# Kernel tuning notes

Hardware: AMD Instinct MI355X
Metric: run time of the kernel (lower is better)

## Reference

```python
import jax, jax.numpy as jnp
import numpy as np

TOP_K = 2
EPS = 1e-10


def setup_inputs() -> dict:
    key = jax.random.key(0)
    k1, k2 = jax.random.split(key)
    B, S, D, E = 4, 4096, 4096, 64
    hidden_states = jax.random.normal(k1, (B, S, D), dtype=jnp.float32)
    # router weight, scaled like a standard linear init
    w_router = jax.random.normal(k2, (D, E), dtype=jnp.float32) / np.sqrt(D)
    return {"hidden_states": hidden_states, "w_router": w_router}


def reference(hidden_states, w_router):
    # router: [B,S,D] x [D,E] -> [B,S,E]
    router_logits = jnp.einsum("bsd,de->bse", hidden_states, w_router)
    # balanced_assignment: softmax, global load, penalty, adjusted top-k
    routing_probs = jax.nn.softmax(router_logits, axis=-1)
    current_load = routing_probs.sum(axis=(0, 1))            # [E]
    load_penalty = current_load / (current_load.mean() + EPS)  # [E]
    adjusted_logits = router_logits - jnp.log(load_penalty + EPS)
    _, expert_indices = jax.lax.top_k(adjusted_logits, TOP_K)  # [B,S,top_k]
    return adjusted_logits, expert_indices
```

## Files before the change

kernel.cpp:

```cpp
#include <hip/hip_runtime.h>
#include <math.h>

#define ROWS 16384
#define DD   4096
#define EE   64
#define EPSF 1e-10f

#define BM     128
#define KT     32
#define KSPLIT 4
#define KRANGE (DD / KSPLIT)
#define NKT    (KRANGE / KT)
#define HPAD   36

typedef __attribute__((ext_vector_type(8))) short short8;
typedef __attribute__((ext_vector_type(4))) float f32x4;

__device__ __forceinline__ short rne_bf16(float f) {
  unsigned u = __float_as_uint(f);
  return (short)((u + 0x7fffu + ((u >> 16) & 1u)) >> 16);
}
__device__ __forceinline__ float bf2f(short s) {
  return __uint_as_float(((unsigned)(unsigned short)s) << 16);
}
__device__ __forceinline__ void split3(float f, short& s0, short& s1,
                                       short& s2) {
  s0 = rne_bf16(f);
  float r1 = f - bf2f(s0);
  s1 = rne_bf16(r1);
  s2 = rne_bf16(r1 - bf2f(s1));
}

__global__ __launch_bounds__(256) void k_gemm(
    const float* __restrict__ h, const float* __restrict__ wr,
    float* __restrict__ logits) {
  __shared__ alignas(16) float hs[2][BM * HPAD];
  __shared__ alignas(16) short wsf[2][3][4][64][8];

  const int t = threadIdx.x;
  const int lane = t & 63;
  const int wv = t >> 6;
  const int row0 = (blockIdx.x >> 2) * BM;
  const int kb0 = (blockIdx.x & 3) * KRANGE;

  f32x4 acc[2][4] = {};

  const int hr = t >> 3;
  const int hk = (t & 7) * 4;
  const int we = lane;
  const int wq = wv;

  float4 hpf[4];
  float wpf[8];

  {
    const float* hp = h + (size_t)(row0 + hr) * DD + kb0 + hk;
#pragma unroll
    for (int i = 0; i < 4; ++i)
      hpf[i] = *(const float4*)(hp + (size_t)32 * i * DD);
    const float* wp = wr + (size_t)(kb0 + wq * 8) * EE + we;
#pragma unroll
    for (int j = 0; j < 8; ++j) wpf[j] = wp[(size_t)j * EE];
  }

  for (int kt = 0; kt < NKT; ++kt) {
    const int buf = kt & 1;
    __syncthreads();
#pragma unroll
    for (int i = 0; i < 4; ++i)
      *(float4*)&hs[buf][(hr + 32 * i) * HPAD + hk] = hpf[i];
    {
      short8 p0, p1, p2;
#pragma unroll
      for (int j = 0; j < 8; ++j) {
        short a, b, c;
        split3(wpf[j], a, b, c);
        p0[j] = a; p1[j] = b; p2[j] = c;
      }
      const int lp = wq * 16 + (we & 15);
      const int et = we >> 4;
      *(short8*)&wsf[buf][0][et][lp][0] = p0;
      *(short8*)&wsf[buf][1][et][lp][0] = p1;
      *(short8*)&wsf[buf][2][et][lp][0] = p2;
    }
    if (kt + 1 < NKT) {
      const int kb = kb0 + (kt + 1) * KT;
      const float* hp = h + (size_t)(row0 + hr) * DD + kb + hk;
#pragma unroll
      for (int i = 0; i < 4; ++i)
        hpf[i] = *(const float4*)(hp + (size_t)32 * i * DD);
      const float* wp = wr + (size_t)(kb + wq * 8) * EE + we;
#pragma unroll
      for (int j = 0; j < 8; ++j) wpf[j] = wp[(size_t)j * EE];
    }
    __syncthreads();

    short8 bf[3][4];
#pragma unroll
    for (int p = 0; p < 3; ++p)
#pragma unroll
      for (int et = 0; et < 4; ++et)
        bf[p][et] = *(const short8*)&wsf[buf][p][et][lane][0];

#pragma unroll
    for (int mt = 0; mt < 2; ++mt) {
      const int rl = wv * 32 + mt * 16 + (lane & 15);
      const float* ap = &hs[buf][rl * HPAD + (lane >> 4) * 8];
      float4 a0 = *(const float4*)ap;
      float4 a1 = *(const float4*)(ap + 4);
      float af[8] = {a0.x, a0.y, a0.z, a0.w, a1.x, a1.y, a1.z, a1.w};
      short8 ah0, ah1, ah2;
#pragma unroll
      for (int j = 0; j < 8; ++j) {
        short a, b, c;
        split3(af[j], a, b, c);
        ah0[j] = a; ah1[j] = b; ah2[j] = c;
      }
#pragma unroll
      for (int et = 0; et < 4; ++et) {
        f32x4 c = acc[mt][et];
        c = __builtin_amdgcn_mfma_f32_16x16x32_bf16(ah0, bf[0][et], c, 0, 0, 0);
        c = __builtin_amdgcn_mfma_f32_16x16x32_bf16(ah0, bf[1][et], c, 0, 0, 0);
        c = __builtin_amdgcn_mfma_f32_16x16x32_bf16(ah1, bf[0][et], c, 0, 0, 0);
        c = __builtin_amdgcn_mfma_f32_16x16x32_bf16(ah0, bf[2][et], c, 0, 0, 0);
        c = __builtin_amdgcn_mfma_f32_16x16x32_bf16(ah1, bf[1][et], c, 0, 0, 0);
        c = __builtin_amdgcn_mfma_f32_16x16x32_bf16(ah2, bf[0][et], c, 0, 0, 0);
        acc[mt][et] = c;
      }
    }
  }

#pragma unroll
  for (int mt = 0; mt < 2; ++mt) {
    const int rbase = row0 + wv * 32 + mt * 16 + (lane >> 4) * 4;
    const int col = lane & 15;
#pragma unroll
    for (int et = 0; et < 4; ++et) {
#pragma unroll
      for (int r = 0; r < 4; ++r)
        atomicAdd(&logits[(size_t)(rbase + r) * EE + et * 16 + col],
                  acc[mt][et][r]);
    }
  }
}

__global__ __launch_bounds__(256) void k_softload(
    const float* __restrict__ logits, float* __restrict__ g_load) {
  __shared__ float red[4][64];
  const int lane = threadIdx.x & 63;
  const int wv = threadIdx.x >> 6;
  float accp = 0.f;
#pragma unroll 4
  for (int i = 0; i < 32; ++i) {
    int row = blockIdx.x * 128 + wv * 32 + i;
    float x = logits[(size_t)row * EE + lane];
    float m = x;
#pragma unroll
    for (int off = 32; off > 0; off >>= 1) m = fmaxf(m, __shfl_xor(m, off, 64));
    float p = __expf(x - m);
    float s = p;
#pragma unroll
    for (int off = 32; off > 0; off >>= 1) s += __shfl_xor(s, off, 64);
    accp += p / s;
  }
  red[wv][lane] = accp;
  __syncthreads();
  if (wv == 0) {
    float s = red[0][lane] + red[1][lane] + red[2][lane] + red[3][lane];
    atomicAdd(&g_load[lane], s);
  }
}

__global__ void k_penalty(const float* __restrict__ g_load,
                          float* __restrict__ g_lp) {
  int t = threadIdx.x;
  float v = g_load[t];
  float s = v;
#pragma unroll
  for (int off = 32; off > 0; off >>= 1) s += __shfl_xor(s, off, 64);
  float mean = s * (1.f / 64.f);
  g_lp[t] = logf(v / (mean + EPSF) + EPSF);
}

__global__ __launch_bounds__(256) void k_top2(float* __restrict__ logits,
                                              const float* __restrict__ g_lp,
                                              float* __restrict__ idx_out) {
  int t = threadIdx.x;
  int lane = t & 63;
  int wv = t >> 6;
  int row = blockIdx.x * 4 + wv;
  size_t base = (size_t)row * EE;

  float a = logits[base + lane] - g_lp[lane];
  logits[base + lane] = a;

  float v = a;
  int idx = lane;
#pragma unroll
  for (int off = 32; off > 0; off >>= 1) {
    float ov = __shfl_xor(v, off, 64);
    int oi = __shfl_xor(idx, off, 64);
    if (ov > v || (ov == v && oi < idx)) { v = ov; idx = oi; }
  }
  int i1 = idx;

  float a2 = (lane == i1) ? -INFINITY : a;
  v = a2;
  idx = lane;
#pragma unroll
  for (int off = 32; off > 0; off >>= 1) {
    float ov = __shfl_xor(v, off, 64);
    int oi = __shfl_xor(idx, off, 64);
    if (ov > v || (ov == v && oi < idx)) { v = ov; idx = oi; }
  }
  int i2 = idx;

  if (lane == 0) {
    idx_out[(size_t)row * 2 + 0] = (float)i1;
    idx_out[(size_t)row * 2 + 1] = (float)i2;
  }
}

extern "C" void kernel_launch(void* const* d_in, const int* in_sizes, int n_in,
                              void* d_out, int out_size, void* d_ws,
                              size_t ws_size, hipStream_t stream) {
  const float* h = (const float*)d_in[0];
  const float* wr = (const float*)d_in[1];
  float* out = (float*)d_out;
  float* logits = out;
  float* idx_out = out + (size_t)ROWS * EE;
  float* g_load = (float*)d_ws;
  float* g_lp = g_load + 64;

  hipMemsetAsync(d_out, 0, (size_t)ROWS * EE * sizeof(float), stream);
  hipMemsetAsync(d_ws, 0, 128 * sizeof(float), stream);
  k_gemm<<<(ROWS / BM) * KSPLIT, 256, 0, stream>>>(h, wr, logits);
  k_softload<<<ROWS / 128, 256, 0, stream>>>(logits, g_load);
  k_penalty<<<1, 64, 0, stream>>>(g_load, g_lp);
  k_top2<<<ROWS / 4, 256, 0, stream>>>(logits, g_lp, idx_out);
}
```

Measured before the change: 426.5 us.

## Pre-split router weights once, DMA them to LDS, load activations directly to registers

A new pre-pass kernel splits the router weights into three bf16 parts once and stores them in a workspace in the MFMA-ready layout. The GEMM kernel then copies those tiles into LDS with global_load_lds instead of re-splitting the weights in every block. Activations are read straight from global memory into registers in the MFMA operand layout, which drops the LDS staging for activations and one barrier per K step. The separate penalty kernel is folded into top2, and softload now runs on smaller blocks. In exchange there is an extra launch plus workspace traffic, and the direct activation loads are less coalesced.

```diff
diff --git a/kernel.cpp b/kernel.cpp
--- a/kernel.cpp
+++ b/kernel.cpp
@@ -11,31 +11,65 @@
 #define KSPLIT 4
 #define KRANGE (DD / KSPLIT)
 #define NKT    (KRANGE / KT)
-#define HPAD   36
+#define WTILE  12288
 
 typedef __attribute__((ext_vector_type(8))) short short8;
 typedef __attribute__((ext_vector_type(4))) float f32x4;
-
-__device__ __forceinline__ short rne_bf16(float f) {
-  unsigned u = __float_as_uint(f);
-  return (short)((u + 0x7fffu + ((u >> 16) & 1u)) >> 16);
-}
-__device__ __forceinline__ float bf2f(short s) {
-  return __uint_as_float(((unsigned)(unsigned short)s) << 16);
-}
-__device__ __forceinline__ void split3(float f, short& s0, short& s1,
-                                       short& s2) {
-  s0 = rne_bf16(f);
-  float r1 = f - bf2f(s0);
-  s1 = rne_bf16(r1);
-  s2 = rne_bf16(r1 - bf2f(s1));
+typedef __attribute__((ext_vector_type(4))) unsigned u32x4;
+
+__device__ __forceinline__ void split3x8(const float f[8], u32x4& w0,
+                                         u32x4& w1, u32x4& w2) {
+#pragma unroll
+  for (int i = 0; i < 4; ++i) {
+    float fa = f[2 * i], fb = f[2 * i + 1];
+    unsigned ua = __float_as_uint(fa), ub = __float_as_uint(fb);
+    unsigned ra = ua + 0x7fffu + ((ua >> 16) & 1u);
+    unsigned rb = ub + 0x7fffu + ((ub >> 16) & 1u);
+    w0[i] = (rb & 0xffff0000u) | (ra >> 16);
+    fa -= __uint_as_float(ra & 0xffff0000u);
+    fb -= __uint_as_float(rb & 0xffff0000u);
+    ua = __float_as_uint(fa); ub = __float_as_uint(fb);
+    ra = ua + 0x7fffu + ((ua >> 16) & 1u);
+    rb = ub + 0x7fffu + ((ub >> 16) & 1u);
+    w1[i] = (rb & 0xffff0000u) | (ra >> 16);
+    fa -= __uint_as_float(ra & 0xffff0000u);
+    fb -= __uint_as_float(rb & 0xffff0000u);
+    ua = __float_as_uint(fa); ub = __float_as_uint(fb);
+    ra = ua + 0x7fffu + ((ua >> 16) & 1u);
+    rb = ub + 0x7fffu + ((ub >> 16) & 1u);
+    w2[i] = (rb & 0xffff0000u) | (ra >> 16);
+  }
+}
+
+__device__ __forceinline__ void dma16(const void* g, void* l) {
+  __builtin_amdgcn_global_load_lds(
+      (const __attribute__((address_space(1))) unsigned int*)g,
+      (__attribute__((address_space(3))) unsigned int*)l, 16, 0, 0);
+}
+
+__global__ __launch_bounds__(256) void k_wsplit(const float* __restrict__ wr,
+                                                unsigned char* __restrict__ out) {
+  const int kt = blockIdx.x;
+  const int t = threadIdx.x;
+  const int lane = t & 63, wv = t >> 6;
+  float f[8];
+  const float* wp = wr + (size_t)(kt * 32 + wv * 8) * EE + lane;
+#pragma unroll
+  for (int j = 0; j < 8; ++j) f[j] = wp[(size_t)j * EE];
+  u32x4 w0, w1, w2;
+  split3x8(f, w0, w1, w2);
+  const int et = lane >> 4;
+  const int lp = wv * 16 + (lane & 15);
+  unsigned char* base = out + (size_t)kt * WTILE + et * 1024 + lp * 16;
+  *(u32x4*)(base + 0 * 4096) = w0;
+  *(u32x4*)(base + 1 * 4096) = w1;
+  *(u32x4*)(base + 2 * 4096) = w2;
 }
 
 __global__ __launch_bounds__(256) void k_gemm(
-    const float* __restrict__ h, const float* __restrict__ wr,
+    const float* __restrict__ h, const unsigned char* __restrict__ wsp,
     float* __restrict__ logits) {
-  __shared__ alignas(16) float hs[2][BM * HPAD];
-  __shared__ alignas(16) short wsf[2][3][4][64][8];
+  __shared__ alignas(16) unsigned char wsf[2][WTILE];
 
   const int t = threadIdx.x;
   const int lane = t & 63;
@@ -45,77 +79,58 @@
 
   f32x4 acc[2][4] = {};
 
-  const int hr = t >> 3;
-  const int hk = (t & 7) * 4;
-  const int we = lane;
-  const int wq = wv;
-
-  float4 hpf[4];
-  float wpf[8];
-
-  {
-    const float* hp = h + (size_t)(row0 + hr) * DD + kb0 + hk;
-#pragma unroll
-    for (int i = 0; i < 4; ++i)
-      hpf[i] = *(const float4*)(hp + (size_t)32 * i * DD);
-    const float* wp = wr + (size_t)(kb0 + wq * 8) * EE + we;
-#pragma unroll
-    for (int j = 0; j < 8; ++j) wpf[j] = wp[(size_t)j * EE];
-  }
+  const int rl0 = row0 + wv * 32 + (lane & 15);
+  const int kcol = kb0 + (lane >> 4) * 8;
+  const float* ap0 = h + (size_t)rl0 * DD + kcol;
+  const float* ap1 = ap0 + (size_t)16 * DD;
+
+  const unsigned char* wsrc = wsp + (size_t)(kb0 / KT) * WTILE;
+  const int chunkoff = wv * 1024 + lane * 16;
+
+  float4 cur[4], nxt[4];
+  cur[0] = *(const float4*)(ap0);
+  cur[1] = *(const float4*)(ap0 + 4);
+  cur[2] = *(const float4*)(ap1);
+  cur[3] = *(const float4*)(ap1 + 4);
+#pragma unroll
+  for (int c = 0; c < 3; ++c)
+    dma16(wsrc + c * 4096 + chunkoff, &wsf[0][c * 4096 + chunkoff]);
 
   for (int kt = 0; kt < NKT; ++kt) {
     const int buf = kt & 1;
+    asm volatile("s_waitcnt vmcnt(0)" ::: "memory");
     __syncthreads();
-#pragma unroll
-    for (int i = 0; i < 4; ++i)
-      *(float4*)&hs[buf][(hr + 32 * i) * HPAD + hk] = hpf[i];
-    {
-      short8 p0, p1, p2;
-#pragma unroll
-      for (int j = 0; j < 8; ++j) {
-        short a, b, c;
-        split3(wpf[j], a, b, c);
-        p0[j] = a; p1[j] = b; p2[j] = c;
-      }
-      const int lp = wq * 16 + (we & 15);
-      const int et = we >> 4;
-      *(short8*)&wsf[buf][0][et][lp][0] = p0;
-      *(short8*)&wsf[buf][1][et][lp][0] = p1;
-      *(short8*)&wsf[buf][2][et][lp][0] = p2;
-    }
+
     if (kt + 1 < NKT) {
-      const int kb = kb0 + (kt + 1) * KT;
-      const float* hp = h + (size_t)(row0 + hr) * DD + kb + hk;
-#pragma unroll
-      for (int i = 0; i < 4; ++i)
-        hpf[i] = *(const float4*)(hp + (size_t)32 * i * DD);
-      const float* wp = wr + (size_t)(kb + wq * 8) * EE + we;
-#pragma unroll
-      for (int j = 0; j < 8; ++j) wpf[j] = wp[(size_t)j * EE];
-    }
-    __syncthreads();
+      const float* p0 = ap0 + (size_t)(kt + 1) * KT;
+      const float* p1 = ap1 + (size_t)(kt + 1) * KT;
+      nxt[0] = *(const float4*)(p0);
+      nxt[1] = *(const float4*)(p0 + 4);
+      nxt[2] = *(const float4*)(p1);
+      nxt[3] = *(const float4*)(p1 + 4);
+      const unsigned char* ws = wsrc + (size_t)(kt + 1) * WTILE;
+#pragma unroll
+      for (int c = 0; c < 3; ++c)
+        dma16(ws + c * 4096 + chunkoff, &wsf[buf ^ 1][c * 4096 + chunkoff]);
+    }
 
     short8 bf[3][4];
 #pragma unroll
     for (int p = 0; p < 3; ++p)
 #pragma unroll
       for (int et = 0; et < 4; ++et)
-        bf[p][et] = *(const short8*)&wsf[buf][p][et][lane][0];
+        bf[p][et] =
+            *(const short8*)&wsf[buf][p * 4096 + et * 1024 + lane * 16];
 
 #pragma unroll
     for (int mt = 0; mt < 2; ++mt) {
-      const int rl = wv * 32 + mt * 16 + (lane & 15);
-      const float* ap = &hs[buf][rl * HPAD + (lane >> 4) * 8];
-      float4 a0 = *(const float4*)ap;
-      float4 a1 = *(const float4*)(ap + 4);
-      float af[8] = {a0.x, a0.y, a0.z, a0.w, a1.x, a1.y, a1.z, a1.w};
-      short8 ah0, ah1, ah2;
-#pragma unroll
-      for (int j = 0; j < 8; ++j) {
-        short a, b, c;
-        split3(af[j], a, b, c);
-        ah0[j] = a; ah1[j] = b; ah2[j] = c;
-      }
+      const float4 a0 = cur[mt * 2], a1 = cur[mt * 2 + 1];
+      const float af[8] = {a0.x, a0.y, a0.z, a0.w, a1.x, a1.y, a1.z, a1.w};
+      u32x4 q0, q1, q2;
+      split3x8(af, q0, q1, q2);
+      const short8 ah0 = __builtin_bit_cast(short8, q0);
+      const short8 ah1 = __builtin_bit_cast(short8, q1);
+      const short8 ah2 = __builtin_bit_cast(short8, q2);
 #pragma unroll
       for (int et = 0; et < 4; ++et) {
         f32x4 c = acc[mt][et];
@@ -128,6 +143,11 @@
         acc[mt][et] = c;
       }
     }
+
+    if (kt + 1 < NKT) {
+#pragma unroll
+      for (int i = 0; i < 4; ++i) cur[i] = nxt[i];
+    }
   }
 
 #pragma unroll
@@ -151,8 +171,8 @@
   const int wv = threadIdx.x >> 6;
   float accp = 0.f;
 #pragma unroll 4
-  for (int i = 0; i < 32; ++i) {
-    int row = blockIdx.x * 128 + wv * 32 + i;
+  for (int i = 0; i < 16; ++i) {
+    int row = blockIdx.x * 64 + wv * 16 + i;
     float x = logits[(size_t)row * EE + lane];
     float m = x;
 #pragma unroll
@@ -171,27 +191,22 @@
   }
 }
 
-__global__ void k_penalty(const float* __restrict__ g_load,
-                          float* __restrict__ g_lp) {
-  int t = threadIdx.x;
-  float v = g_load[t];
-  float s = v;
-#pragma unroll
-  for (int off = 32; off > 0; off >>= 1) s += __shfl_xor(s, off, 64);
-  float mean = s * (1.f / 64.f);
-  g_lp[t] = logf(v / (mean + EPSF) + EPSF);
-}
-
 __global__ __launch_bounds__(256) void k_top2(float* __restrict__ logits,
-                                              const float* __restrict__ g_lp,
+                                              const float* __restrict__ g_load,
                                               float* __restrict__ idx_out) {
   int t = threadIdx.x;
   int lane = t & 63;
   int wv = t >> 6;
   int row = blockIdx.x * 4 + wv;
+
+  float v0 = g_load[lane];
+  float s0 = v0;
+#pragma unroll
+  for (int off = 32; off > 0; off >>= 1) s0 += __shfl_xor(s0, off, 64);
+  float lp = logf(v0 / (s0 * (1.f / 64.f) + EPSF) + EPSF);
+
   size_t base = (size_t)row * EE;
-
-  float a = logits[base + lane] - g_lp[lane];
+  float a = logits[base + lane] - lp;
   logits[base + lane] = a;
 
   float v = a;
@@ -230,12 +245,12 @@
   float* logits = out;
   float* idx_out = out + (size_t)ROWS * EE;
   float* g_load = (float*)d_ws;
-  float* g_lp = g_load + 64;
+  unsigned char* wsp = (unsigned char*)d_ws + 512;
 
   hipMemsetAsync(d_out, 0, (size_t)ROWS * EE * sizeof(float), stream);
-  hipMemsetAsync(d_ws, 0, 128 * sizeof(float), stream);
-  k_gemm<<<(ROWS / BM) * KSPLIT, 256, 0, stream>>>(h, wr, logits);
-  k_softload<<<ROWS / 128, 256, 0, stream>>>(logits, g_load);
-  k_penalty<<<1, 64, 0, stream>>>(g_load, g_lp);
-  k_top2<<<ROWS / 4, 256, 0, stream>>>(logits, g_lp, idx_out);
-}
+  hipMemsetAsync(d_ws, 0, 512, stream);
+  k_wsplit<<<DD / KT, 256, 0, stream>>>(wr, wsp);
+  k_gemm<<<(ROWS / BM) * KSPLIT, 256, 0, stream>>>(h, wsp, logits);
+  k_softload<<<ROWS / 64, 256, 0, stream>>>(logits, g_load);
+  k_top2<<<ROWS / 4, 256, 0, stream>>>(logits, g_load, idx_out);
+}
```

After: 420.1 us. About the same (-1.5%).
